# Kernel optimization log

Measured on AMD Instinct MI355X. Metric: run time of the kernel, lower is better.

Reference implementation:

```python
import jax, jax.numpy as jnp
import numpy as np

E, W, C, N, Q = 8, 5, 640, 49, 75


def setup_inputs() -> dict:
    key = jax.random.key(0)
    k1, k2 = jax.random.split(key)
    proto = jax.random.normal(k1, (E, W, C, 1, N), dtype=jnp.float32)
    query = jax.random.normal(k2, (E, Q, C, 1, N), dtype=jnp.float32)
    return {"proto": proto, "query": query}


def reference(proto, query):
    # proto: [E, W, C, 1, N] -> [E, W, C, N]; query: [E, Q, C, 1, N] -> [E, Q, C, N]
    p = jnp.squeeze(proto, axis=3)
    q = jnp.squeeze(query, axis=3)
    # cosine similarity map over channel dim C:
    # sim[e,q,w,n,m] = <p[e,w,:,n], q[e,q,:,m]>
    sim = jnp.einsum('ewcn,eqcm->eqwnm', p, q)
    norm_p = jnp.linalg.norm(p, axis=2)  # [E, W, N]
    norm_q = jnp.linalg.norm(q, axis=2)  # [E, Q, N]
    denom = norm_p[:, None, :, :, None] * norm_q[:, :, None, None, :] + 1e-8
    return sim / denom  # [E, Q, W, N, N]
```

## Files before the change

kernel.cpp:

```cpp
#include <hip/hip_runtime.h>
#include <hip/hip_bf16.h>


#define E_CNT 8
#define W_CNT 5
#define C_CNT 640
#define N_CNT 49
#define Q_CNT 75
#define MROWS 245
#define NC32 20
#define AFRAG_CH 16384
#define AIMG_E (NC32 * AFRAG_CH)
#define AIMG_SIZE (E_CNT * AIMG_E)
#define PN_OFF AIMG_SIZE
#define PN_BYTES (E_CNT * 10 * MROWS * 4)
#define WS1 ((size_t)(PN_OFF + PN_BYTES))

typedef __attribute__((ext_vector_type(8))) short bf16x8;
typedef __attribute__((ext_vector_type(4))) float f32x4;

static __device__ __forceinline__ short f2bf(float f) {
    __hip_bfloat16 h = __float2bfloat16(f);
    return *reinterpret_cast<short*>(&h);
}

__global__ __launch_bounds__(256, 4)
void prep_a_kernel(const float* __restrict__ proto,
                   unsigned char* __restrict__ aimg,
                   float* __restrict__ pn_part)
{
    __shared__ float pns[MROWS];
    const int b = blockIdx.x;
    const int e = b / 10, c64 = b % 10;
    const float* pbase = proto + (size_t)e * (W_CNT * C_CNT * N_CNT);
    unsigned char* ebase = aimg + (size_t)e * AIMG_E;
    const int t = threadIdx.x;
    if (t < MROWS) pns[t] = 0.f;
    __syncthreads();

    #pragma unroll
    for (int i = 0; i < 8; ++i) {
        const int s = t + i * 256;
        int nw, kb;
        bf16x8 pk;
        if (s < 8 * MROWS) {
            kb = s / MROWS;
            nw = s - kb * MROWS;
            const int w = nw / N_CNT, n = nw - w * N_CNT;
            const float* g = pbase + ((size_t)(w * C_CNT + c64 * 64 + kb * 8)) * N_CNT + n;
            float ss = 0.f;
            #pragma unroll
            for (int j = 0; j < 8; ++j) {
                const float f = g[(size_t)j * N_CNT];
                ss += f * f;
                pk[j] = f2bf(f);
            }
            atomicAdd(&pns[nw], ss);
        } else {
            const int x = s - 8 * MROWS;
            nw = MROWS + (x >> 3);
            kb = x & 7;
            pk = (bf16x8){0, 0, 0, 0, 0, 0, 0, 0};
        }
        const int c32 = c64 * 2 + (kb >> 2);
        const int ln2 = ((kb & 3) << 4) | (nw & 15);
        *reinterpret_cast<bf16x8*>(
            ebase + (size_t)c32 * AFRAG_CH + (size_t)((nw >> 4) * 64 + ln2) * 16) = pk;
    }
    __syncthreads();
    if (t < MROWS) pn_part[(size_t)(e * 10 + c64) * MROWS + t] = pns[t];
}

__global__ __launch_bounds__(256, 4)
void gemm6_kernel(const float* __restrict__ query,
                  const unsigned char* __restrict__ aimg,
                  const float* __restrict__ pn_part,
                  float* __restrict__ out)
{
    __shared__ __align__(16) unsigned char Bbuf[2 * 4096];
    __shared__ float qn[64];
    __shared__ float pnl[128];

    const int b = blockIdx.x;
    const int e = b & 7;
    const int mh = (b >> 3) & 1;
    const int q = b >> 4;
    const int eq = e * Q_CNT + q;
    const int t = threadIdx.x;
    const int wv = t >> 6, ln = t & 63;
    const int lrow = ln & 15, lk = ln >> 4;

    const float* __restrict__ qsl = query + (size_t)eq * (C_CNT * N_CNT);

    const int scol = wv * 16 + lrow;
    const int scolc = (scol < N_CNT) ? scol : (N_CNT - 1);
    const float* __restrict__ sbase = qsl + (size_t)(lk * 8) * N_CNT + scolc;
    const int swoff = wv * 1024 + ln * 16;

    const int rt0 = mh * 8 + wv * 2;
    const unsigned char* __restrict__ abase =
        aimg + (size_t)e * AIMG_E + (size_t)(rt0 * 64 + ln) * 16;

    if (t < 128) {
        const int row = mh * 128 + t;
        float s = 0.f;
        if (row < MROWS) {
            #pragma unroll
            for (int cc = 0; cc < 10; ++cc)
                s += pn_part[(size_t)(e * 10 + cc) * MROWS + row];
        }
        pnl[t] = sqrtf(s);
    }

    float vB[2][8];
    bf16x8 afr[2][2];
    f32x4 acc[2][4];
    #pragma unroll
    for (int i = 0; i < 2; ++i)
        #pragma unroll
        for (int j = 0; j < 4; ++j) acc[i][j] = (f32x4){0.f, 0.f, 0.f, 0.f};
    float ssq = 0.f;

#define G6_BARRIER() asm volatile("s_waitcnt lgkmcnt(0)\n\ts_barrier" ::: "memory")

#define G6_BISSUE(c, s_) do {                                                   \
    _Pragma("unroll")                                                           \
    for (int j_ = 0; j_ < 8; ++j_)                                              \
        vB[s_][j_] = sbase[(size_t)((c) * 32 + j_) * N_CNT];                    \
} while (0)

#define G6_AISSUE(c, s_) do {                                                   \
    _Pragma("unroll")                                                           \
    for (int fi_ = 0; fi_ < 2; ++fi_)                                           \
        afr[s_][fi_] = *reinterpret_cast<const bf16x8*>(                        \
            abase + (size_t)(c) * AFRAG_CH + fi_ * 1024);                       \
} while (0)

#define G6_CVTW(s_, buf) do {                                                   \
    bf16x8 pk_;                                                                 \
    _Pragma("unroll")                                                           \
    for (int j_ = 0; j_ < 8; ++j_) {                                            \
        const float f_ = vB[s_][j_]; ssq += f_ * f_; pk_[j_] = f2bf(f_);        \
    }                                                                           \
    *reinterpret_cast<bf16x8*>(Bbuf + (buf) * 4096 + swoff) = pk_;              \
} while (0)

    G6_BISSUE(0, 0);
    G6_AISSUE(0, 0);
    G6_BISSUE(1, 1);
    G6_CVTW(0, 0);
    G6_BARRIER();

    #pragma unroll
    for (int c = 0; c < NC32; ++c) {
        if (c + 2 < NC32) G6_BISSUE(c + 2, c & 1);
        if (c + 1 < NC32) G6_AISSUE(c + 1, (c + 1) & 1);

        {
            const unsigned char* bb = Bbuf + (c & 1) * 4096;
            bf16x8 bfr[4];
            #pragma unroll
            for (int fj = 0; fj < 4; ++fj)
                bfr[fj] = *reinterpret_cast<const bf16x8*>(bb + fj * 1024 + ln * 16);
            #pragma unroll
            for (int fi = 0; fi < 2; ++fi)
                #pragma unroll
                for (int fj = 0; fj < 4; ++fj)
                    acc[fi][fj] = __builtin_amdgcn_mfma_f32_16x16x32_bf16(
                        afr[c & 1][fi], bfr[fj], acc[fi][fj], 0, 0, 0);
        }

        if (c + 1 < NC32) {
            G6_CVTW((c + 1) & 1, (c + 1) & 1);
            G6_BARRIER();
        }
    }

    {
        float s = ssq;
        s += __shfl_xor(s, 16);
        s += __shfl_xor(s, 32);
        if (lk == 0) qn[wv * 16 + lrow] = s;
    }
    __syncthreads();

    float nq4[4];
    #pragma unroll
    for (int fj = 0; fj < 4; ++fj) {
        const int m = fj * 16 + lrow;
        nq4[fj] = (m < N_CNT) ? sqrtf(qn[m]) : 1.f;
    }
    float* __restrict__ osl = out + (size_t)eq * (W_CNT * N_CNT * N_CNT);
    #pragma unroll
    for (int fi = 0; fi < 2; ++fi) {
        #pragma unroll
        for (int rr = 0; rr < 4; ++rr) {
            const int lr = wv * 32 + fi * 16 + lk * 4 + rr;
            const int row = mh * 128 + lr;
            if (row < MROWS) {
                const float np_ = pnl[lr];
                #pragma unroll
                for (int fj = 0; fj < 4; ++fj) {
                    const int m = fj * 16 + lrow;
                    if (m < N_CNT) {
                        const float den = np_ * nq4[fj] + 1e-8f;
                        osl[row * N_CNT + m] = acc[fi][fj][rr] * __builtin_amdgcn_rcpf(den);
                    }
                }
            }
        }
    }
#undef G6_BARRIER
#undef G6_BISSUE
#undef G6_AISSUE
#undef G6_CVTW
}

struct SMemFB {
    unsigned char A[256 * 128];
    unsigned char B[64 * 128];
    float ns[320];
};

__global__ __launch_bounds__(512, 4)
void sim_fallback_kernel(const float* __restrict__ proto,
                         const float* __restrict__ query,
                         float* __restrict__ out)
{
    __shared__ SMemFB smf;
    const int t = threadIdx.x;
    const int e = blockIdx.x / Q_CNT;
    const int q = blockIdx.x - e * Q_CNT;
    const float* pbase = proto + (size_t)e * (W_CNT * C_CNT * N_CNT);
    const float* qbase = query + ((size_t)e * Q_CNT + q) * (C_CNT * N_CNT);
    unsigned char* lds = (unsigned char*)&smf;
    if (t < 320) smf.ns[t] = 0.f;
    if (t < 208) {
        if (t < 88) *reinterpret_cast<f32x4*>(smf.A + 245 * 128 + t * 16) = (f32x4){0.f,0.f,0.f,0.f};
        else        *reinterpret_cast<f32x4*>(smf.B + 49 * 128 + (t - 88) * 16) = (f32x4){0.f,0.f,0.f,0.f};
    }
    const int nslot5 = (t < 304);
    const float* gp[5];
    int offidx[5];
    #pragma unroll
    for (int i = 0; i < 5; ++i) {
        gp[i] = pbase; offidx[i] = 0;
        if (i < 4 || nslot5) {
            const int s = t + i * 512;
            if (s < 1960) {
                const int kb = s / 245, nw = s - kb * 245;
                const int w = nw / 49, n = nw - w * 49;
                gp[i] = pbase + ((size_t)w * C_CNT + kb * 8) * N_CNT + n;
                offidx[i] = (nw * 128 + ((kb ^ (nw & 7)) << 4)) | (nw << 16);
            } else {
                const int s2 = s - 1960;
                const int kb = s2 / 49, mq = s2 - kb * 49;
                gp[i] = qbase + (size_t)(kb * 8) * N_CNT + mq;
                offidx[i] = (32768 + mq * 128 + ((kb ^ (mq & 7)) << 4)) | ((256 + mq) << 16);
            }
        }
    }
    float v[5][8];
    float ss[5] = {0.f,0.f,0.f,0.f,0.f};
    #pragma unroll
    for (int i = 0; i < 4; ++i)
        #pragma unroll
        for (int j = 0; j < 8; ++j) v[i][j] = gp[i][(size_t)j * N_CNT];
    if (nslot5)
        #pragma unroll
        for (int j = 0; j < 8; ++j) v[4][j] = gp[4][(size_t)j * N_CNT];
    f32x4 acc[2][4];
    #pragma unroll
    for (int i = 0; i < 2; ++i)
        #pragma unroll
        for (int j = 0; j < 4; ++j) acc[i][j] = (f32x4){0.f,0.f,0.f,0.f};
    const int wv = t >> 6, ln = t & 63, lrow = ln & 15, lk = ln >> 4;
    for (int kc = 0; kc < 10; ++kc) {
        #pragma unroll
        for (int i = 0; i < 5; ++i) {
            if (i < 4 || nslot5) {
                bf16x8 pk; float s8 = 0.f;
                #pragma unroll
                for (int j = 0; j < 8; ++j) { const float f = v[i][j]; s8 += f*f; pk[j] = f2bf(f); }
                ss[i] += s8;
                *reinterpret_cast<bf16x8*>(lds + (offidx[i] & 0xFFFF)) = pk;
            }
        }
        __syncthreads();
        if (kc < 9) {
            #pragma unroll
            for (int i = 0; i < 4; ++i) {
                gp[i] += 64 * N_CNT;
                #pragma unroll
                for (int j = 0; j < 8; ++j) v[i][j] = gp[i][(size_t)j * N_CNT];
            }
            if (nslot5) {
                gp[4] += 64 * N_CNT;
                #pragma unroll
                for (int j = 0; j < 8; ++j) v[4][j] = gp[4][(size_t)j * N_CNT];
            }
        }
        #pragma unroll
        for (int ks = 0; ks < 2; ++ks) {
            bf16x8 af[2], bfr[4];
            #pragma unroll
            for (int i = 0; i < 2; ++i) {
                const int row = (wv * 2 + i) * 16 + lrow;
                const int gr = (ks * 4 + lk) ^ (row & 7);
                af[i] = *reinterpret_cast<const bf16x8*>(lds + row * 128 + gr * 16);
            }
            #pragma unroll
            for (int j = 0; j < 4; ++j) {
                const int mq = j * 16 + lrow;
                const int gr = (ks * 4 + lk) ^ (mq & 7);
                bfr[j] = *reinterpret_cast<const bf16x8*>(lds + 32768 + mq * 128 + gr * 16);
            }
            #pragma unroll
            for (int i = 0; i < 2; ++i)
                #pragma unroll
                for (int j = 0; j < 4; ++j)
                    acc[i][j] = __builtin_amdgcn_mfma_f32_16x16x32_bf16(af[i], bfr[j], acc[i][j], 0, 0, 0);
        }
        __syncthreads();
    }
    #pragma unroll
    for (int i = 0; i < 5; ++i)
        if (i < 4 || nslot5) atomicAdd(&smf.ns[offidx[i] >> 16], ss[i]);
    __syncthreads();
    float nq[4];
    #pragma unroll
    for (int j = 0; j < 4; ++j) {
        const int mq = j * 16 + lrow;
        nq[j] = (mq < N_CNT) ? sqrtf(smf.ns[256 + mq]) : 1.f;
    }
    float* obase = out + (size_t)(e * Q_CNT + q) * (W_CNT * N_CNT * N_CNT);
    #pragma unroll
    for (int i = 0; i < 2; ++i) {
        #pragma unroll
        for (int rr = 0; rr < 4; ++rr) {
            const int nw = (wv * 2 + i) * 16 + lk * 4 + rr;
            if (nw < W_CNT * N_CNT) {
                const int w = nw / 49, n = nw - w * 49;
                const float np_ = sqrtf(smf.ns[nw]);
                float* orow = obase + ((size_t)w * N_CNT + n) * N_CNT;
                #pragma unroll
                for (int j = 0; j < 4; ++j) {
                    const int mq = j * 16 + lrow;
                    if (mq < N_CNT) orow[mq] = acc[i][j][rr] / (np_ * nq[j] + 1e-8f);
                }
            }
        }
    }
}

extern "C" void kernel_launch(void* const* d_in, const int* in_sizes, int n_in,
                              void* d_out, int out_size, void* d_ws, size_t ws_size,
                              hipStream_t stream)
{
    const float* proto = (const float*)d_in[0];
    const float* query = (const float*)d_in[1];
    float* out = (float*)d_out;

    if (ws_size < WS1) {
        hipLaunchKernelGGL(sim_fallback_kernel, dim3(E_CNT * Q_CNT), dim3(512), 0, stream,
                           proto, query, out);
        return;
    }

    unsigned char* aimg = (unsigned char*)d_ws;
    float* pn_part = (float*)((unsigned char*)d_ws + PN_OFF);

    hipLaunchKernelGGL(prep_a_kernel, dim3(E_CNT * 10), dim3(256), 0, stream,
                       proto, aimg, pn_part);
    hipLaunchKernelGGL(gemm6_kernel, dim3(E_CNT * Q_CNT * 2), dim3(256), 0, stream,
                       query, aimg, pn_part, out);
}
```

Measured before the change: 39.07 us.

## Merge row halves into one 512-thread block sharing staged query tile

```diff
diff --git a/kernel.cpp b/kernel.cpp
--- a/kernel.cpp
+++ b/kernel.cpp
@@ -23,6 +23,8 @@
     __hip_bfloat16 h = __float2bfloat16(f);
     return *reinterpret_cast<short*>(&h);
 }
+
+#define RAW_BARRIER() asm volatile("s_waitcnt lgkmcnt(0)\n\ts_barrier" ::: "memory")
 
 __global__ __launch_bounds__(256, 4)
 void prep_a_kernel(const float* __restrict__ proto,
@@ -71,20 +73,19 @@
     if (t < MROWS) pn_part[(size_t)(e * 10 + c64) * MROWS + t] = pns[t];
 }
 
-__global__ __launch_bounds__(256, 4)
-void gemm6_kernel(const float* __restrict__ query,
+__global__ __launch_bounds__(512, 4)
+void gemm9_kernel(const float* __restrict__ query,
                   const unsigned char* __restrict__ aimg,
                   const float* __restrict__ pn_part,
                   float* __restrict__ out)
 {
     __shared__ __align__(16) unsigned char Bbuf[2 * 4096];
     __shared__ float qn[64];
-    __shared__ float pnl[128];
+    __shared__ float pnl[256];
 
     const int b = blockIdx.x;
     const int e = b & 7;
-    const int mh = (b >> 3) & 1;
-    const int q = b >> 4;
+    const int q = b >> 3;
     const int eq = e * Q_CNT + q;
     const int t = threadIdx.x;
     const int wv = t >> 6, ln = t & 63;
@@ -92,28 +93,29 @@
 
     const float* __restrict__ qsl = query + (size_t)eq * (C_CNT * N_CNT);
 
-    const int scol = wv * 16 + lrow;
+    const bool stg = t < 256;
+    const int fjS = (t >> 6) & 3;
+    const int lnS = t & 63;
+    const int scol = fjS * 16 + (t & 15);
     const int scolc = (scol < N_CNT) ? scol : (N_CNT - 1);
-    const float* __restrict__ sbase = qsl + (size_t)(lk * 8) * N_CNT + scolc;
-    const int swoff = wv * 1024 + ln * 16;
-
-    const int rt0 = mh * 8 + wv * 2;
+    const int lkS = (t >> 4) & 3;
+    const float* __restrict__ sbase = qsl + (size_t)(lkS * 8) * N_CNT + scolc;
+    const int swoff = fjS * 1024 + lnS * 16;
+
     const unsigned char* __restrict__ abase =
-        aimg + (size_t)e * AIMG_E + (size_t)(rt0 * 64 + ln) * 16;
-
-    if (t < 128) {
-        const int row = mh * 128 + t;
+        aimg + (size_t)e * AIMG_E + (size_t)((wv * 2) * 64 + ln) * 16;
+
+    if (t < MROWS) {
         float s = 0.f;
-        if (row < MROWS) {
-            #pragma unroll
-            for (int cc = 0; cc < 10; ++cc)
-                s += pn_part[(size_t)(e * 10 + cc) * MROWS + row];
-        }
+        #pragma unroll
+        for (int cc = 0; cc < 10; ++cc)
+            s += pn_part[(size_t)(e * 10 + cc) * MROWS + t];
         pnl[t] = sqrtf(s);
     }
 
-    float vB[2][8];
-    bf16x8 afr[2][2];
+    float vBA0, vBA1, vBA2, vBA3, vBA4, vBA5, vBA6, vBA7;
+    float vBB0, vBB1, vBB2, vBB3, vBB4, vBB5, vBB6, vBB7;
+    bf16x8 afrA0, afrA1, afrB0, afrB1;
     f32x4 acc[2][4];
     #pragma unroll
     for (int i = 0; i < 2; ++i)
@@ -121,58 +123,82 @@
         for (int j = 0; j < 4; ++j) acc[i][j] = (f32x4){0.f, 0.f, 0.f, 0.f};
     float ssq = 0.f;
 
-#define G6_BARRIER() asm volatile("s_waitcnt lgkmcnt(0)\n\ts_barrier" ::: "memory")
-
-#define G6_BISSUE(c, s_) do {                                                   \
-    _Pragma("unroll")                                                           \
-    for (int j_ = 0; j_ < 8; ++j_)                                              \
-        vB[s_][j_] = sbase[(size_t)((c) * 32 + j_) * N_CNT];                    \
+#define BISSUE_A(c) do { if (stg) {                                             \
+    const size_t k0_ = (size_t)(c) * 32 * N_CNT;                                \
+    vBA0 = sbase[k0_];              vBA1 = sbase[k0_ + 1 * N_CNT];              \
+    vBA2 = sbase[k0_ + 2 * N_CNT];  vBA3 = sbase[k0_ + 3 * N_CNT];              \
+    vBA4 = sbase[k0_ + 4 * N_CNT];  vBA5 = sbase[k0_ + 5 * N_CNT];              \
+    vBA6 = sbase[k0_ + 6 * N_CNT];  vBA7 = sbase[k0_ + 7 * N_CNT]; } } while (0)
+
+#define BISSUE_B(c) do { if (stg) {                                             \
+    const size_t k0_ = (size_t)(c) * 32 * N_CNT;                                \
+    vBB0 = sbase[k0_];              vBB1 = sbase[k0_ + 1 * N_CNT];              \
+    vBB2 = sbase[k0_ + 2 * N_CNT];  vBB3 = sbase[k0_ + 3 * N_CNT];              \
+    vBB4 = sbase[k0_ + 4 * N_CNT];  vBB5 = sbase[k0_ + 5 * N_CNT];              \
+    vBB6 = sbase[k0_ + 6 * N_CNT];  vBB7 = sbase[k0_ + 7 * N_CNT]; } } while (0)
+
+#define CVTW_A(bufofs) do { if (stg) {                                          \
+    bf16x8 pk_;                                                                 \
+    ssq += vBA0*vBA0 + vBA1*vBA1 + vBA2*vBA2 + vBA3*vBA3                        \
+         + vBA4*vBA4 + vBA5*vBA5 + vBA6*vBA6 + vBA7*vBA7;                       \
+    pk_[0]=f2bf(vBA0); pk_[1]=f2bf(vBA1); pk_[2]=f2bf(vBA2); pk_[3]=f2bf(vBA3); \
+    pk_[4]=f2bf(vBA4); pk_[5]=f2bf(vBA5); pk_[6]=f2bf(vBA6); pk_[7]=f2bf(vBA7); \
+    *reinterpret_cast<bf16x8*>(Bbuf + (bufofs) + swoff) = pk_; } } while (0)
+
+#define CVTW_B(bufofs) do { if (stg) {                                          \
+    bf16x8 pk_;                                                                 \
+    ssq += vBB0*vBB0 + vBB1*vBB1 + vBB2*vBB2 + vBB3*vBB3                        \
+         + vBB4*vBB4 + vBB5*vBB5 + vBB6*vBB6 + vBB7*vBB7;                       \
+    pk_[0]=f2bf(vBB0); pk_[1]=f2bf(vBB1); pk_[2]=f2bf(vBB2); pk_[3]=f2bf(vBB3); \
+    pk_[4]=f2bf(vBB4); pk_[5]=f2bf(vBB5); pk_[6]=f2bf(vBB6); pk_[7]=f2bf(vBB7); \
+    *reinterpret_cast<bf16x8*>(Bbuf + (bufofs) + swoff) = pk_; } } while (0)
+
+#define AISSUE_A(c) do {                                                        \
+    afrA0 = *reinterpret_cast<const bf16x8*>(abase + (size_t)(c) * AFRAG_CH);   \
+    afrA1 = *reinterpret_cast<const bf16x8*>(abase + (size_t)(c) * AFRAG_CH + 1024); \
 } while (0)
 
-#define G6_AISSUE(c, s_) do {                                                   \
-    _Pragma("unroll")                                                           \
-    for (int fi_ = 0; fi_ < 2; ++fi_)                                           \
-        afr[s_][fi_] = *reinterpret_cast<const bf16x8*>(                        \
-            abase + (size_t)(c) * AFRAG_CH + fi_ * 1024);                       \
+#define AISSUE_B(c) do {                                                        \
+    afrB0 = *reinterpret_cast<const bf16x8*>(abase + (size_t)(c) * AFRAG_CH);   \
+    afrB1 = *reinterpret_cast<const bf16x8*>(abase + (size_t)(c) * AFRAG_CH + 1024); \
 } while (0)
 
-#define G6_CVTW(s_, buf) do {                                                   \
-    bf16x8 pk_;                                                                 \
-    _Pragma("unroll")                                                           \
-    for (int j_ = 0; j_ < 8; ++j_) {                                            \
-        const float f_ = vB[s_][j_]; ssq += f_ * f_; pk_[j_] = f2bf(f_);        \
-    }                                                                           \
-    *reinterpret_cast<bf16x8*>(Bbuf + (buf) * 4096 + swoff) = pk_;              \
+#define DO_MFMA(a0, a1, bufofs) do {                                            \
+    bf16x8 bfr0_ = *reinterpret_cast<const bf16x8*>(Bbuf + (bufofs) + 0 * 1024 + ln * 16); \
+    bf16x8 bfr1_ = *reinterpret_cast<const bf16x8*>(Bbuf + (bufofs) + 1 * 1024 + ln * 16); \
+    bf16x8 bfr2_ = *reinterpret_cast<const bf16x8*>(Bbuf + (bufofs) + 2 * 1024 + ln * 16); \
+    bf16x8 bfr3_ = *reinterpret_cast<const bf16x8*>(Bbuf + (bufofs) + 3 * 1024 + ln * 16); \
+    acc[0][0] = __builtin_amdgcn_mfma_f32_16x16x32_bf16(a0, bfr0_, acc[0][0], 0, 0, 0); \
+    acc[0][1] = __builtin_amdgcn_mfma_f32_16x16x32_bf16(a0, bfr1_, acc[0][1], 0, 0, 0); \
+    acc[0][2] = __builtin_amdgcn_mfma_f32_16x16x32_bf16(a0, bfr2_, acc[0][2], 0, 0, 0); \
+    acc[0][3] = __builtin_amdgcn_mfma_f32_16x16x32_bf16(a0, bfr3_, acc[0][3], 0, 0, 0); \
+    acc[1][0] = __builtin_amdgcn_mfma_f32_16x16x32_bf16(a1, bfr0_, acc[1][0], 0, 0, 0); \
+    acc[1][1] = __builtin_amdgcn_mfma_f32_16x16x32_bf16(a1, bfr1_, acc[1][1], 0, 0, 0); \
+    acc[1][2] = __builtin_amdgcn_mfma_f32_16x16x32_bf16(a1, bfr2_, acc[1][2], 0, 0, 0); \
+    acc[1][3] = __builtin_amdgcn_mfma_f32_16x16x32_bf16(a1, bfr3_, acc[1][3], 0, 0, 0); \
 } while (0)
 
-    G6_BISSUE(0, 0);
-    G6_AISSUE(0, 0);
-    G6_BISSUE(1, 1);
-    G6_CVTW(0, 0);
-    G6_BARRIER();
-
-    #pragma unroll
-    for (int c = 0; c < NC32; ++c) {
-        if (c + 2 < NC32) G6_BISSUE(c + 2, c & 1);
-        if (c + 1 < NC32) G6_AISSUE(c + 1, (c + 1) & 1);
-
-        {
-            const unsigned char* bb = Bbuf + (c & 1) * 4096;
-            bf16x8 bfr[4];
-            #pragma unroll
-            for (int fj = 0; fj < 4; ++fj)
-                bfr[fj] = *reinterpret_cast<const bf16x8*>(bb + fj * 1024 + ln * 16);
-            #pragma unroll
-            for (int fi = 0; fi < 2; ++fi)
-                #pragma unroll
-                for (int fj = 0; fj < 4; ++fj)
-                    acc[fi][fj] = __builtin_amdgcn_mfma_f32_16x16x32_bf16(
-                        afr[c & 1][fi], bfr[fj], acc[fi][fj], 0, 0, 0);
-        }
-
-        if (c + 1 < NC32) {
-            G6_CVTW((c + 1) & 1, (c + 1) & 1);
-            G6_BARRIER();
+    BISSUE_A(0);
+    AISSUE_A(0);
+    BISSUE_B(1);
+    CVTW_A(0);
+    RAW_BARRIER();
+
+    for (int cc = 0; cc < NC32; cc += 2) {
+        const bool lastpair = (cc == NC32 - 2);
+        if (!lastpair) BISSUE_A(cc + 2);
+        AISSUE_B(cc + 1);
+        DO_MFMA(afrA0, afrA1, 0);
+        CVTW_B(4096);
+        RAW_BARRIER();
+        if (!lastpair) {
+            BISSUE_B(cc + 3);
+            AISSUE_A(cc + 2);
+        }
+        DO_MFMA(afrB0, afrB1, 4096);
+        if (!lastpair) {
+            CVTW_A(0);
+            RAW_BARRIER();
         }
     }
 
@@ -180,7 +206,7 @@
         float s = ssq;
         s += __shfl_xor(s, 16);
         s += __shfl_xor(s, 32);
-        if (lk == 0) qn[wv * 16 + lrow] = s;
+        if (stg && lkS == 0) qn[fjS * 16 + (t & 15)] = s;
     }
     __syncthreads();
 
@@ -195,10 +221,9 @@
     for (int fi = 0; fi < 2; ++fi) {
         #pragma unroll
         for (int rr = 0; rr < 4; ++rr) {
-            const int lr = wv * 32 + fi * 16 + lk * 4 + rr;
-            const int row = mh * 128 + lr;
+            const int row = wv * 32 + fi * 16 + lk * 4 + rr;
             if (row < MROWS) {
-                const float np_ = pnl[lr];
+                const float np_ = pnl[row];
                 #pragma unroll
                 for (int fj = 0; fj < 4; ++fj) {
                     const int m = fj * 16 + lrow;
@@ -210,10 +235,13 @@
             }
         }
     }
-#undef G6_BARRIER
-#undef G6_BISSUE
-#undef G6_AISSUE
-#undef G6_CVTW
+#undef BISSUE_A
+#undef BISSUE_B
+#undef CVTW_A
+#undef CVTW_B
+#undef AISSUE_A
+#undef AISSUE_B
+#undef DO_MFMA
 }
 
 struct SMemFB {
@@ -372,6 +400,6 @@
 
     hipLaunchKernelGGL(prep_a_kernel, dim3(E_CNT * 10), dim3(256), 0, stream,
                        proto, aimg, pn_part);
-    hipLaunchKernelGGL(gemm6_kernel, dim3(E_CNT * Q_CNT * 2), dim3(256), 0, stream,
+    hipLaunchKernelGGL(gemm9_kernel, dim3(E_CNT * Q_CNT), dim3(512), 0, stream,
                        query, aimg, pn_part, out);
 }
```

Measured after the change: 42.94 us. 9.9% more time.

## Stage query chunks through LDS with coalesced vector loads and a deeper pipeline

Applied to the files above, without the earlier changes.

```diff
diff --git a/kernel.cpp b/kernel.cpp
--- a/kernel.cpp
+++ b/kernel.cpp
@@ -9,6 +9,7 @@
 #define Q_CNT 75
 #define MROWS 245
 #define NC32 20
+#define CHF 1568
 #define AFRAG_CH 16384
 #define AIMG_E (NC32 * AFRAG_CH)
 #define AIMG_SIZE (E_CNT * AIMG_E)
@@ -23,6 +24,8 @@
     __hip_bfloat16 h = __float2bfloat16(f);
     return *reinterpret_cast<short*>(&h);
 }
+
+#define RAW_BARRIER() asm volatile("s_waitcnt lgkmcnt(0)\n\ts_barrier" ::: "memory")
 
 __global__ __launch_bounds__(256, 4)
 void prep_a_kernel(const float* __restrict__ proto,
@@ -71,12 +74,13 @@
     if (t < MROWS) pn_part[(size_t)(e * 10 + c64) * MROWS + t] = pns[t];
 }
 
-__global__ __launch_bounds__(256, 4)
-void gemm6_kernel(const float* __restrict__ query,
-                  const unsigned char* __restrict__ aimg,
-                  const float* __restrict__ pn_part,
-                  float* __restrict__ out)
+__global__ __launch_bounds__(256, 2)
+void gemm11_kernel(const float* __restrict__ query,
+                   const unsigned char* __restrict__ aimg,
+                   const float* __restrict__ pn_part,
+                   float* __restrict__ out)
 {
+    __shared__ __align__(16) float fbuf[3][CHF];
     __shared__ __align__(16) unsigned char Bbuf[2 * 4096];
     __shared__ float qn[64];
     __shared__ float pnl[128];
@@ -90,17 +94,22 @@
     const int wv = t >> 6, ln = t & 63;
     const int lrow = ln & 15, lk = ln >> 4;
 
-    const float* __restrict__ qsl = query + (size_t)eq * (C_CNT * N_CNT);
-
-    const int scol = wv * 16 + lrow;
+    const f32x4* __restrict__ qsl4 =
+        reinterpret_cast<const f32x4*>(query + (size_t)eq * (C_CNT * N_CNT));
+
+    const int fjS = t >> 6;
+    const int scol = fjS * 16 + (t & 15);
     const int scolc = (scol < N_CNT) ? scol : (N_CNT - 1);
-    const float* __restrict__ sbase = qsl + (size_t)(lk * 8) * N_CNT + scolc;
-    const int swoff = wv * 1024 + ln * 16;
-
-    const int rt0 = mh * 8 + wv * 2;
+    const int lkS = (t >> 4) & 3;
+    const int swoff = fjS * 1024 + (t & 63) * 16;
+    const int frd0 = lkS * 8 * N_CNT + scolc;
+
+    const bool t2 = t < (CHF / 4 - 256);
+
     const unsigned char* __restrict__ abase =
-        aimg + (size_t)e * AIMG_E + (size_t)(rt0 * 64 + ln) * 16;
-
+        aimg + (size_t)e * AIMG_E + (size_t)((mh * 8 + wv * 2) * 64 + ln) * 16;
+
+    if (t < 64) qn[t] = 0.f;
     if (t < 128) {
         const int row = mh * 128 + t;
         float s = 0.f;
@@ -112,8 +121,8 @@
         pnl[t] = sqrtf(s);
     }
 
-    float vB[2][8];
-    bf16x8 afr[2][2];
+    f32x4 vqA0, vqA1, vqB0, vqB1;
+    bf16x8 afrA0, afrA1, afrB0, afrB1;
     f32x4 acc[2][4];
     #pragma unroll
     for (int i = 0; i < 2; ++i)
@@ -121,66 +130,95 @@
         for (int j = 0; j < 4; ++j) acc[i][j] = (f32x4){0.f, 0.f, 0.f, 0.f};
     float ssq = 0.f;
 
-#define G6_BARRIER() asm volatile("s_waitcnt lgkmcnt(0)\n\ts_barrier" ::: "memory")
-
-#define G6_BISSUE(c, s_) do {                                                   \
-    _Pragma("unroll")                                                           \
-    for (int j_ = 0; j_ < 8; ++j_)                                              \
-        vB[s_][j_] = sbase[(size_t)((c) * 32 + j_) * N_CNT];                    \
-} while (0)
-
-#define G6_AISSUE(c, s_) do {                                                   \
-    _Pragma("unroll")                                                           \
-    for (int fi_ = 0; fi_ < 2; ++fi_)                                           \
-        afr[s_][fi_] = *reinterpret_cast<const bf16x8*>(                        \
-            abase + (size_t)(c) * AFRAG_CH + fi_ * 1024);                       \
-} while (0)
-
-#define G6_CVTW(s_, buf) do {                                                   \
+#define GLOAD_A(c) do {                                                         \
+    vqA0 = qsl4[(size_t)(c) * (CHF / 4) + t];                                   \
+    if (t2) vqA1 = qsl4[(size_t)(c) * (CHF / 4) + 256 + t];                     \
+} while (0)
+#define GLOAD_B(c) do {                                                         \
+    vqB0 = qsl4[(size_t)(c) * (CHF / 4) + t];                                   \
+    if (t2) vqB1 = qsl4[(size_t)(c) * (CHF / 4) + 256 + t];                     \
+} while (0)
+#define FWRITE_A(c) do {                                                        \
+    float* d_ = fbuf[(c) % 3];                                                  \
+    *reinterpret_cast<f32x4*>(d_ + t * 4) = vqA0;                               \
+    if (t2) *reinterpret_cast<f32x4*>(d_ + 1024 + t * 4) = vqA1;                \
+} while (0)
+#define FWRITE_B(c) do {                                                        \
+    float* d_ = fbuf[(c) % 3];                                                  \
+    *reinterpret_cast<f32x4*>(d_ + t * 4) = vqB0;                               \
+    if (t2) *reinterpret_cast<f32x4*>(d_ + 1024 + t * 4) = vqB1;                \
+} while (0)
+#define CVT(c) do {                                                             \
+    const float* f_ = fbuf[(c) % 3];                                            \
+    float v0_ = f_[frd0];               float v1_ = f_[frd0 + 1 * N_CNT];       \
+    float v2_ = f_[frd0 + 2 * N_CNT];   float v3_ = f_[frd0 + 3 * N_CNT];       \
+    float v4_ = f_[frd0 + 4 * N_CNT];   float v5_ = f_[frd0 + 5 * N_CNT];       \
+    float v6_ = f_[frd0 + 6 * N_CNT];   float v7_ = f_[frd0 + 7 * N_CNT];       \
+    ssq += v0_*v0_ + v1_*v1_ + v2_*v2_ + v3_*v3_                                \
+         + v4_*v4_ + v5_*v5_ + v6_*v6_ + v7_*v7_;                               \
     bf16x8 pk_;                                                                 \
-    _Pragma("unroll")                                                           \
-    for (int j_ = 0; j_ < 8; ++j_) {                                            \
-        const float f_ = vB[s_][j_]; ssq += f_ * f_; pk_[j_] = f2bf(f_);        \
-    }                                                                           \
-    *reinterpret_cast<bf16x8*>(Bbuf + (buf) * 4096 + swoff) = pk_;              \
-} while (0)
-
-    G6_BISSUE(0, 0);
-    G6_AISSUE(0, 0);
-    G6_BISSUE(1, 1);
-    G6_CVTW(0, 0);
-    G6_BARRIER();
-
-    #pragma unroll
+    pk_[0]=f2bf(v0_); pk_[1]=f2bf(v1_); pk_[2]=f2bf(v2_); pk_[3]=f2bf(v3_);     \
+    pk_[4]=f2bf(v4_); pk_[5]=f2bf(v5_); pk_[6]=f2bf(v6_); pk_[7]=f2bf(v7_);     \
+    *reinterpret_cast<bf16x8*>(Bbuf + ((c) & 1) * 4096 + swoff) = pk_;          \
+} while (0)
+#define AISSUE_A(c) do {                                                        \
+    afrA0 = *reinterpret_cast<const bf16x8*>(abase + (size_t)(c) * AFRAG_CH);   \
+    afrA1 = *reinterpret_cast<const bf16x8*>(abase + (size_t)(c) * AFRAG_CH + 1024); \
+} while (0)
+#define AISSUE_B(c) do {                                                        \
+    afrB0 = *reinterpret_cast<const bf16x8*>(abase + (size_t)(c) * AFRAG_CH);   \
+    afrB1 = *reinterpret_cast<const bf16x8*>(abase + (size_t)(c) * AFRAG_CH + 1024); \
+} while (0)
+#define DO_MFMA(c, a0, a1) do {                                                 \
+    const unsigned char* bb_ = Bbuf + ((c) & 1) * 4096;                         \
+    bf16x8 bfr0_ = *reinterpret_cast<const bf16x8*>(bb_ + 0 * 1024 + ln * 16);  \
+    bf16x8 bfr1_ = *reinterpret_cast<const bf16x8*>(bb_ + 1 * 1024 + ln * 16);  \
+    bf16x8 bfr2_ = *reinterpret_cast<const bf16x8*>(bb_ + 2 * 1024 + ln * 16);  \
+    bf16x8 bfr3_ = *reinterpret_cast<const bf16x8*>(bb_ + 3 * 1024 + ln * 16);  \
+    acc[0][0] = __builtin_amdgcn_mfma_f32_16x16x32_bf16(a0, bfr0_, acc[0][0], 0, 0, 0); \
+    acc[0][1] = __builtin_amdgcn_mfma_f32_16x16x32_bf16(a0, bfr1_, acc[0][1], 0, 0, 0); \
+    acc[0][2] = __builtin_amdgcn_mfma_f32_16x16x32_bf16(a0, bfr2_, acc[0][2], 0, 0, 0); \
+    acc[0][3] = __builtin_amdgcn_mfma_f32_16x16x32_bf16(a0, bfr3_, acc[0][3], 0, 0, 0); \
+    acc[1][0] = __builtin_amdgcn_mfma_f32_16x16x32_bf16(a1, bfr0_, acc[1][0], 0, 0, 0); \
+    acc[1][1] = __builtin_amdgcn_mfma_f32_16x16x32_bf16(a1, bfr1_, acc[1][1], 0, 0, 0); \
+    acc[1][2] = __builtin_amdgcn_mfma_f32_16x16x32_bf16(a1, bfr2_, acc[1][2], 0, 0, 0); \
+    acc[1][3] = __builtin_amdgcn_mfma_f32_16x16x32_bf16(a1, bfr3_, acc[1][3], 0, 0, 0); \
+} while (0)
+
+    GLOAD_A(0);
+    GLOAD_B(1);
+    FWRITE_A(0);
+    AISSUE_A(0);
+    RAW_BARRIER();
+    CVT(0);
+    GLOAD_A(2);
+    FWRITE_B(1);
+    AISSUE_B(1);
+    RAW_BARRIER();
+
     for (int c = 0; c < NC32; ++c) {
-        if (c + 2 < NC32) G6_BISSUE(c + 2, c & 1);
-        if (c + 1 < NC32) G6_AISSUE(c + 1, (c + 1) & 1);
-
-        {
-            const unsigned char* bb = Bbuf + (c & 1) * 4096;
-            bf16x8 bfr[4];
-            #pragma unroll
-            for (int fj = 0; fj < 4; ++fj)
-                bfr[fj] = *reinterpret_cast<const bf16x8*>(bb + fj * 1024 + ln * 16);
-            #pragma unroll
-            for (int fi = 0; fi < 2; ++fi)
-                #pragma unroll
-                for (int fj = 0; fj < 4; ++fj)
-                    acc[fi][fj] = __builtin_amdgcn_mfma_f32_16x16x32_bf16(
-                        afr[c & 1][fi], bfr[fj], acc[fi][fj], 0, 0, 0);
-        }
-
-        if (c + 1 < NC32) {
-            G6_CVTW((c + 1) & 1, (c + 1) & 1);
-            G6_BARRIER();
-        }
+        if (c + 3 < NC32) {
+            if (c & 1) GLOAD_A(c + 3); else GLOAD_B(c + 3);
+        }
+        if (c + 2 < NC32) {
+            if (c & 1) FWRITE_B(c + 2); else FWRITE_A(c + 2);
+        }
+        if (c + 1 < NC32) CVT(c + 1);
+        if (c & 1) {
+            DO_MFMA(c, afrB0, afrB1);
+            if (c + 2 < NC32) AISSUE_B(c + 2);
+        } else {
+            DO_MFMA(c, afrA0, afrA1);
+            if (c + 2 < NC32) AISSUE_A(c + 2);
+        }
+        if (c + 1 < NC32) RAW_BARRIER();
     }
 
     {
         float s = ssq;
         s += __shfl_xor(s, 16);
         s += __shfl_xor(s, 32);
-        if (lk == 0) qn[wv * 16 + lrow] = s;
+        if (lkS == 0) qn[fjS * 16 + (t & 15)] = s;
     }
     __syncthreads();
 
@@ -210,10 +248,14 @@
             }
         }
     }
-#undef G6_BARRIER
-#undef G6_BISSUE
-#undef G6_AISSUE
-#undef G6_CVTW
+#undef GLOAD_A
+#undef GLOAD_B
+#undef FWRITE_A
+#undef FWRITE_B
+#undef CVT
+#undef AISSUE_A
+#undef AISSUE_B
+#undef DO_MFMA
 }
 
 struct SMemFB {
@@ -372,6 +414,6 @@
 
     hipLaunchKernelGGL(prep_a_kernel, dim3(E_CNT * 10), dim3(256), 0, stream,
                        proto, aimg, pn_part);
-    hipLaunchKernelGGL(gemm6_kernel, dim3(E_CNT * Q_CNT * 2), dim3(256), 0, stream,
+    hipLaunchKernelGGL(gemm11_kernel, dim3(E_CNT * Q_CNT * 2), dim3(256), 0, stream,
                        query, aimg, pn_part, out);
 }
```

Result: slower. 46.36 us (+18.7%).
